# Kernel tuning notes

Hardware: AMD Instinct MI355X
Metric: run time of the kernel (lower is better)

The kernel has to match this reference:

```python
import jax, jax.numpy as jnp
import numpy as np

D_MODEL, N_HEAD, D_HEAD = 1024, 16, 64
BATCH, Q_LEN = 2, 2048
LN_EPS = 1e-5


def _rel_shift(x):
    # x: [b, q, k, n] -- standard Transformer-XL relative shift
    b, q, k, n = x.shape
    zero_pad = jnp.zeros((b, q, 1, n), dtype=x.dtype)
    x_padded = jnp.concatenate([zero_pad, x], axis=2)      # [b, q, k+1, n]
    x_padded = x_padded.reshape(b, k + 1, q, n)
    return x_padded[:, 1:].reshape(b, q, k, n)


def _layer_norm(x, gamma, beta):
    mu = jnp.mean(x, axis=-1, keepdims=True)
    var = jnp.mean(jnp.square(x - mu), axis=-1, keepdims=True)
    return (x - mu) * jax.lax.rsqrt(var + LN_EPS) * gamma + beta


def setup_inputs() -> dict:
    key = jax.random.key(0)
    ks = jax.random.split(key, 8)
    inp = {
        "x": jax.random.normal(ks[0], (BATCH, Q_LEN, D_MODEL), jnp.float32),
        "relative_pos": jax.random.normal(ks[1], (Q_LEN, D_MODEL), jnp.float32),
        "r_w_bias": jax.random.normal(ks[2], (N_HEAD, D_HEAD), jnp.float32) * 0.02,
        "r_r_bias": jax.random.normal(ks[3], (N_HEAD, D_HEAD), jnp.float32) * 0.02,
        "attn_mask": jax.random.randint(ks[4], (BATCH, Q_LEN), 0, 2).astype(bool),
        "W_qkv": jax.random.normal(ks[5], (D_MODEL, 3 * N_HEAD * D_HEAD), jnp.float32) / np.sqrt(D_MODEL),
        "W_rel": jax.random.normal(ks[6], (D_MODEL, N_HEAD * D_HEAD), jnp.float32) / np.sqrt(D_MODEL),
        "W_out": jax.random.normal(ks[7], (N_HEAD * D_HEAD, D_MODEL), jnp.float32) / np.sqrt(N_HEAD * D_HEAD),
        "ln_gamma": jnp.ones((D_MODEL,), jnp.float32),
        "ln_beta": jnp.zeros((D_MODEL,), jnp.float32),
    }
    return inp


def reference(x, relative_pos, r_w_bias, r_r_bias, attn_mask, W_qkv, W_rel, W_out, ln_gamma, ln_beta):
    b, q_len, _ = x.shape
    r_len = relative_pos.shape[0]
    scale = 1.0 / np.sqrt(D_HEAD)

    w_heads = x @ W_qkv                                    # [b, q, 3*n*d]
    w_q, w_k, w_v = jnp.split(w_heads, 3, axis=-1)
    k_len = w_k.shape[1]

    w_q = w_q.reshape(b, q_len, N_HEAD, D_HEAD)
    w_k = w_k.reshape(b, k_len, N_HEAD, D_HEAD)
    w_v = w_v.reshape(b, k_len, N_HEAD, D_HEAD)
    r_k = (relative_pos @ W_rel).reshape(r_len, N_HEAD, D_HEAD)

    rw_q = w_q + r_w_bias                                  # [b, q, n, d]
    rr_q = w_q + r_r_bias

    ac = jnp.einsum('bind,bjnd->bijn', rw_q, w_k)          # content score
    bd = jnp.einsum('bind,jnd->bijn', rr_q, r_k)           # position score
    bd = _rel_shift(bd)

    attn_score = (ac + bd) * scale                         # [b, q, k, n]
    attn_score = jnp.where(attn_mask[:, None, :, None], -jnp.inf, attn_score)
    attn_prob = jax.nn.softmax(attn_score, axis=2)

    context = jnp.einsum('bijn,bjnd->bind', attn_prob, w_v)
    context = context.reshape(b, q_len, N_HEAD * D_HEAD)
    attn_out = context @ W_out
    return _layer_norm(x + attn_out, ln_gamma, ln_beta)
```

## Files before the change

### kernel.cpp

```cpp
#include <hip/hip_runtime.h>
#include <hip/hip_bf16.h>
#include <math.h>

#define S_LEN 2048
#define NHEAD 16
#define DHEAD 64
#define DMODEL 1024
#define NBATCH 2

typedef unsigned short u16;
typedef __attribute__((ext_vector_type(8))) short bf16x8;
typedef __attribute__((ext_vector_type(4))) short short4v;
typedef __attribute__((ext_vector_type(4))) float f32x4;

__device__ __forceinline__ short f2bs(float x) {
    __hip_bfloat16 h = __float2bfloat16(x);
    return __builtin_bit_cast(short, h);
}

#define GL2LDS(g, l)                                                         \
    __builtin_amdgcn_global_load_lds(                                        \
        (const __attribute__((address_space(1))) void*)(g),                  \
        (__attribute__((address_space(3))) void*)(l), 16, 0, 0)

__global__ __launch_bounds__(256) void cast_f32_bf16(const float* __restrict__ in,
                                                     u16* __restrict__ out) {
    const int i = (blockIdx.x * 256 + threadIdx.x) * 4;
    float4 v = *(const float4*)(in + i);
    short4v t;
    t[0] = f2bs(v.x); t[1] = f2bs(v.y); t[2] = f2bs(v.z); t[3] = f2bs(v.w);
    *(short4v*)(out + i) = t;
}

__global__ __launch_bounds__(256) void transp_cast(const float* __restrict__ W,
                                                   u16* __restrict__ Wt,
                                                   int K, int N) {
    __shared__ float t[64][65];
    const int k0 = blockIdx.y * 64, n0 = blockIdx.x * 64;
    const int r = threadIdx.x >> 4;
    const int c4 = (threadIdx.x & 15) * 4;
    #pragma unroll
    for (int it = 0; it < 4; ++it) {
        float4 v = *(const float4*)(W + (size_t)(k0 + it * 16 + r) * N + n0 + c4);
        t[c4 + 0][it * 16 + r] = v.x;
        t[c4 + 1][it * 16 + r] = v.y;
        t[c4 + 2][it * 16 + r] = v.z;
        t[c4 + 3][it * 16 + r] = v.w;
    }
    __syncthreads();
    #pragma unroll
    for (int it = 0; it < 4; ++it) {
        const int nn = it * 16 + r;
        short4v o;
        o[0] = f2bs(t[nn][c4 + 0]); o[1] = f2bs(t[nn][c4 + 1]);
        o[2] = f2bs(t[nn][c4 + 2]); o[3] = f2bs(t[nn][c4 + 3]);
        *(short4v*)(Wt + (size_t)(n0 + nn) * K + k0 + c4) = o;
    }
}

#define GEMM_BODY(Aptr, Btptr, Kdim)                                          \
    __shared__ u16 As[128 * 64];                                              \
    __shared__ u16 Bs[128 * 64];                                              \
    const int tid = threadIdx.x;                                              \
    const int lane = tid & 63;                                                \
    const int w = tid >> 6;                                                   \
    const int quad = lane >> 4, col = lane & 15;                              \
    const int bm = blockIdx.y * 128, bn = blockIdx.x * 128;                   \
    const int wm = (w >> 1) * 64, wn = (w & 1) * 64;                          \
    f32x4 acc[4][4];                                                          \
    _Pragma("unroll")                                                         \
    for (int mt = 0; mt < 4; ++mt)                                            \
        _Pragma("unroll")                                                     \
        for (int nt = 0; nt < 4; ++nt) acc[mt][nt] = (f32x4){0.f,0.f,0.f,0.f};\
    for (int k0 = 0; k0 < (Kdim); k0 += 64) {                                 \
        _Pragma("unroll")                                                     \
        for (int it = 0; it < 4; ++it) {                                      \
            const int cb = it * 256 + w * 64;                                 \
            const int c = cb + lane;                                          \
            const int r = c >> 3;                                             \
            const int o = ((c & 7) ^ (r & 7)) * 8;                            \
            GL2LDS((Aptr) + (size_t)(bm + r) * (Kdim) + k0 + o, As + (size_t)cb * 8); \
            GL2LDS((Btptr) + (size_t)(bn + r) * (Kdim) + k0 + o, Bs + (size_t)cb * 8);\
        }                                                                     \
        __syncthreads();                                                      \
        _Pragma("unroll")                                                     \
        for (int kc = 0; kc < 2; ++kc) {                                      \
            bf16x8 af[4], bfr[4];                                             \
            _Pragma("unroll")                                                 \
            for (int t = 0; t < 4; ++t) {                                     \
                const int am = wm + t * 16 + col;                             \
                const int aj = kc * 4 + quad;                                 \
                af[t] = *(const bf16x8*)&As[(size_t)am * 64 + ((aj ^ (am & 7)) * 8)]; \
                const int bn2 = wn + t * 16 + col;                            \
                bfr[t] = *(const bf16x8*)&Bs[(size_t)bn2 * 64 + ((aj ^ (bn2 & 7)) * 8)]; \
            }                                                                 \
            _Pragma("unroll")                                                 \
            for (int mt = 0; mt < 4; ++mt)                                    \
                _Pragma("unroll")                                             \
                for (int nt = 0; nt < 4; ++nt)                                \
                    acc[mt][nt] = __builtin_amdgcn_mfma_f32_16x16x32_bf16(    \
                        af[mt], bfr[nt], acc[mt][nt], 0, 0, 0);               \
        }                                                                     \
        __syncthreads();                                                      \
    }

__global__ __launch_bounds__(256, 2) void gemm_qkv(
    const u16* __restrict__ A, const u16* __restrict__ Bt,
    const float* __restrict__ rwb, const float* __restrict__ rrb,
    u16* __restrict__ qrw_b, u16* __restrict__ qrr_b,
    u16* __restrict__ kb, u16* __restrict__ vbT)
{
    GEMM_BODY(A, Bt, DMODEL)
    #pragma unroll
    for (int mt = 0; mt < 4; ++mt) {
        const int row0 = bm + wm + mt * 16 + quad * 4;
        const int b = row0 >> 11;
        const int s0 = row0 & 2047;
        #pragma unroll
        for (int nt = 0; nt < 4; ++nt) {
            const int cn = bn + wn + nt * 16 + col;
            const int sec = cn >> 10;
            const int cc = cn & 1023;
            const int h = cc >> 6, d = cc & 63;
            const int bh = b * NHEAD + h;
            if (sec == 0) {
                const float bw = rwb[cc], br = rrb[cc];
                #pragma unroll
                for (int r = 0; r < 4; ++r) {
                    const size_t o = ((size_t)bh * S_LEN + s0 + r) * 64 + d;
                    qrw_b[o] = (u16)f2bs(acc[mt][nt][r] + bw);
                    qrr_b[o] = (u16)f2bs(acc[mt][nt][r] + br);
                }
            } else if (sec == 1) {
                #pragma unroll
                for (int r = 0; r < 4; ++r)
                    kb[((size_t)bh * S_LEN + s0 + r) * 64 + d] =
                        (u16)f2bs(acc[mt][nt][r]);
            } else {
                short4v t;
                t[0] = f2bs(acc[mt][nt][0]); t[1] = f2bs(acc[mt][nt][1]);
                t[2] = f2bs(acc[mt][nt][2]); t[3] = f2bs(acc[mt][nt][3]);
                *(short4v*)(vbT + ((size_t)bh * 64 + d) * S_LEN + s0) = t;
            }
        }
    }
}

__global__ __launch_bounds__(256, 2) void gemm_rel(
    const u16* __restrict__ A, const u16* __restrict__ Bt,
    u16* __restrict__ rkb)
{
    GEMM_BODY(A, Bt, DMODEL)
    #pragma unroll
    for (int mt = 0; mt < 4; ++mt) {
        const int l0 = bm + wm + mt * 16 + quad * 4;
        #pragma unroll
        for (int nt = 0; nt < 4; ++nt) {
            const int cn = bn + wn + nt * 16 + col;
            const int h = cn >> 6, d = cn & 63;
            #pragma unroll
            for (int r = 0; r < 4; ++r)
                rkb[((size_t)h * S_LEN + l0 + r) * 64 + d] =
                    (u16)f2bs(acc[mt][nt][r]);
        }
    }
}

__global__ __launch_bounds__(256, 2) void gemm_out(
    const u16* __restrict__ A, const u16* __restrict__ Bt,
    float* __restrict__ Cf, int N, int K)
{
    GEMM_BODY(A, Bt, K)
    #pragma unroll
    for (int mt = 0; mt < 4; ++mt)
        #pragma unroll
        for (int nt = 0; nt < 4; ++nt)
            #pragma unroll
            for (int r = 0; r < 4; ++r) {
                const int row = bm + wm + mt * 16 + quad * 4 + r;
                const int cn = bn + wn + nt * 16 + col;
                Cf[(size_t)row * N + cn] = acc[mt][nt][r];
            }
}

__global__ __launch_bounds__(512, 2) void flash_attn(
    const u16* __restrict__ qrw_b, const u16* __restrict__ qrr_b,
    const u16* __restrict__ kb, const u16* __restrict__ vbT,
    const u16* __restrict__ rkb, const int* __restrict__ mask,
    u16* __restrict__ ctxb)
{
    const int lane = threadIdx.x & 63;
    const int w    = threadIdx.x >> 6;
    const int quad = lane >> 4;
    const int col  = lane & 15;
    const int bh   = blockIdx.y;
    const int b    = bh >> 4;
    const int n    = bh & 15;
    const int B0   = blockIdx.x * 128;
    const int iw0  = B0 + w * 16;

    __shared__ u16 Ks[64 * 64];
    __shared__ u16 Vs[64 * 64];
    __shared__ u16 Rs[192 * 64];
    __shared__ u16 Pr[8][16][72];
    __shared__ float madd[S_LEN];

    const size_t headQ = (size_t)bh * S_LEN * 64;
    const size_t headR = (size_t)n  * S_LEN * 64;

    for (int i = threadIdx.x; i < S_LEN; i += 512)
        madd[i] = mask[b * S_LEN + i] ? -16384.f : 0.f;

    bf16x8 a_rw[2], a_rr0[2], a_rr1[2];
    {
        const int r0 = iw0 + col;
        const int r1 = (r0 + 1 < S_LEN) ? (r0 + 1) : (S_LEN - 1);
        #pragma unroll
        for (int kc = 0; kc < 2; ++kc) {
            const int doff = kc * 32 + quad * 8;
            a_rw[kc]  = *(const bf16x8*)(qrw_b + headQ + (size_t)r0 * 64 + doff);
            a_rr0[kc] = *(const bf16x8*)(qrr_b + headQ + (size_t)r0 * 64 + doff);
            a_rr1[kc] = *(const bf16x8*)(qrr_b + headQ + (size_t)r1 * 64 + doff);
        }
    }

    f32x4 O[4];
    float l_acc[4] = {0.f, 0.f, 0.f, 0.f};
    #pragma unroll
    for (int dt = 0; dt < 4; ++dt) O[dt] = (f32x4){0.f, 0.f, 0.f, 0.f};

    const int swz  = ((lane & 7) ^ ((lane >> 3) & 7)) * 8;
    const int lrow = lane >> 3;
    const int csel = col & 7;
    const int delta = B0 - 0 + 16 * w;

    for (int u0 = 0; u0 < S_LEN; u0 += 64) {
        const int dblk = B0 - u0;
        const int dw = dblk + 16 * w;
        const bool mixed = (dw >= 0) && (dw <= 48);
        __syncthreads();
        const int pbase = (dblk >= 0) ? (S_LEN - 128 - dblk) : (-dblk - 129);
        #pragma unroll
        for (int t = 0; t < 5; ++t) {
            const int idx = w * 5 + t;
            if (idx < 8) {
                GL2LDS(kb + headQ + (size_t)(u0 + idx * 8 + lrow) * 64 + swz,
                       Ks + idx * 512);
            } else if (idx < 16) {
                const int c = idx - 8;
                GL2LDS(vbT + ((size_t)bh * 64 + c * 8 + lrow) * S_LEN + u0 + swz,
                       Vs + c * 512);
            } else {
                const int c = idx - 16;
                int rr = pbase + c * 8 + lrow;
                rr = rr < 0 ? 0 : (rr > S_LEN - 1 ? S_LEN - 1 : rr);
                GL2LDS(rkb + headR + (size_t)rr * 64 + swz, Rs + c * 512);
            }
        }
        bf16x8 rf2[5][2];
        if (mixed) {
            #pragma unroll
            for (int g = 0; g < 5; ++g) {
                const int u = g * 16 + col;
                int row = (dblk >= 0) ? (u - dw - 17) : (S_LEN - 16 - dw + u);
                row = row < 0 ? 0 : (row > S_LEN - 1 ? S_LEN - 1 : row);
                const u16* rb = rkb + headR + (size_t)row * 64 + quad * 8;
                rf2[g][0] = *(const bf16x8*)(rb);
                rf2[g][1] = *(const bf16x8*)(rb + 32);
            }
        }
        __syncthreads();

        f32x4 sc[4];
        #pragma unroll
        for (int nt = 0; nt < 4; ++nt) {
            const int m = nt * 16 + col;
            bf16x8 k0 = *(const bf16x8*)&Ks[m * 64 + ((quad ^ csel) * 8)];
            bf16x8 k1 = *(const bf16x8*)&Ks[m * 64 + (((4 + quad) ^ csel) * 8)];
            f32x4 c = (f32x4){0.f, 0.f, 0.f, 0.f};
            c = __builtin_amdgcn_mfma_f32_16x16x32_bf16(a_rw[0], k0, c, 0, 0, 0);
            c = __builtin_amdgcn_mfma_f32_16x16x32_bf16(a_rw[1], k1, c, 0, 0, 0);
            sc[nt] = c;
        }

        f32x4 pnl[5], oth[5];
        {
            const bf16x8* aP = (dblk >= 0) ? a_rr0 : a_rr1;
            #pragma unroll
            for (int g = 0; g < 5; ++g) {
                const int m = g * 16 + col + 112 - 16 * w;
                bf16x8 r0 = *(const bf16x8*)&Rs[m * 64 + ((quad ^ csel) * 8)];
                bf16x8 r1 = *(const bf16x8*)&Rs[m * 64 + (((4 + quad) ^ csel) * 8)];
                f32x4 c = (f32x4){0.f, 0.f, 0.f, 0.f};
                c = __builtin_amdgcn_mfma_f32_16x16x32_bf16(aP[0], r0, c, 0, 0, 0);
                c = __builtin_amdgcn_mfma_f32_16x16x32_bf16(aP[1], r1, c, 0, 0, 0);
                pnl[g] = c;
            }
        }
        #pragma unroll
        for (int g = 0; g < 5; ++g) oth[g] = (f32x4){0.f, 0.f, 0.f, 0.f};
        if (mixed) {
            const bf16x8* aV = (dblk >= 0) ? a_rr1 : a_rr0;
            #pragma unroll
            for (int g = 0; g < 5; ++g) {
                f32x4 c = (f32x4){0.f, 0.f, 0.f, 0.f};
                c = __builtin_amdgcn_mfma_f32_16x16x32_bf16(aV[0], rf2[g][0], c, 0, 0, 0);
                c = __builtin_amdgcn_mfma_f32_16x16x32_bf16(aV[1], rf2[g][1], c, 0, 0, 0);
                oth[g] = c;
            }
        }
        const int lim1 = 15 + dw;
        #pragma unroll
        for (int g = 0; g < 5; ++g) {
            const int u = g * 16 + col;
            #pragma unroll
            for (int r = 0; r < 4; ++r) {
                const float r1v = (dblk >= 0) ? pnl[g][r] : oth[g][r];
                const float r2v = (dblk >= 0) ? oth[g][r] : pnl[g][r];
                pnl[g][r] = (u <= lim1) ? r1v : ((u == lim1 + 1) ? 0.f : r2v);
            }
        }

        #pragma unroll
        for (int nt = 0; nt < 4; ++nt) {
            const float ma = madd[u0 + nt * 16 + col];
            #pragma unroll
            for (int r = 0; r < 4; ++r) {
                const int uo = col + 15 - quad * 4 - r;
                const int src = (quad << 4) | (uo & 15);
                float blo = __shfl(pnl[nt][r], src, 64);
                float bhi = __shfl(pnl[nt + 1][r], src, 64);
                float bd = (uo < 16) ? blo : bhi;
                float p = __expf(fmaf(sc[nt][r] + bd, 0.125f, ma));
                sc[nt][r] = p;
                l_acc[r] += p;
            }
        }

        #pragma unroll
        for (int nt = 0; nt < 4; ++nt)
            #pragma unroll
            for (int r = 0; r < 4; ++r)
                Pr[w][quad * 4 + r][nt * 16 + col] = (u16)f2bs(sc[nt][r]);
        bf16x8 pa[2];
        pa[0] = *(const bf16x8*)&Pr[w][col][quad * 8];
        pa[1] = *(const bf16x8*)&Pr[w][col][32 + quad * 8];

        #pragma unroll
        for (int dt = 0; dt < 4; ++dt) {
            const int m = dt * 16 + col;
            bf16x8 v0 = *(const bf16x8*)&Vs[m * 64 + ((quad ^ csel) * 8)];
            bf16x8 v1 = *(const bf16x8*)&Vs[m * 64 + (((4 + quad) ^ csel) * 8)];
            f32x4 c = O[dt];
            c = __builtin_amdgcn_mfma_f32_16x16x32_bf16(pa[0], v0, c, 0, 0, 0);
            c = __builtin_amdgcn_mfma_f32_16x16x32_bf16(pa[1], v1, c, 0, 0, 0);
            O[dt] = c;
        }
    }

    float inv[4];
    #pragma unroll
    for (int r = 0; r < 4; ++r) {
        float s = l_acc[r];
        #pragma unroll
        for (int off = 1; off < 16; off <<= 1)
            s += __shfl_xor(s, off, 64);
        inv[r] = 1.f / s;
    }
    #pragma unroll
    for (int dt = 0; dt < 4; ++dt)
        #pragma unroll
        for (int r = 0; r < 4; ++r) {
            const int i = iw0 + quad * 4 + r;
            ctxb[((size_t)b * S_LEN + i) * DMODEL + n * 64 + dt * 16 + col] =
                (u16)f2bs(O[dt][r] * inv[r]);
        }
}

__global__ __launch_bounds__(256) void ln_kernel(const float* __restrict__ x,
                                                 const float* __restrict__ ao,
                                                 const float* __restrict__ gamma,
                                                 const float* __restrict__ beta,
                                                 float* __restrict__ out) {
    const int r = blockIdx.x;
    const int tid = threadIdx.x;
    const size_t base = (size_t)r * DMODEL + tid * 4;
    float4 xv = *(const float4*)(x + base);
    float4 av = *(const float4*)(ao + base);
    float v0 = xv.x + av.x, v1 = xv.y + av.y, v2 = xv.z + av.z, v3 = xv.w + av.w;

    float s = v0 + v1 + v2 + v3;
    #pragma unroll
    for (int off = 32; off > 0; off >>= 1) s += __shfl_xor(s, off, 64);
    __shared__ float red[4];
    __shared__ float red2[4];
    if ((tid & 63) == 0) red[tid >> 6] = s;
    __syncthreads();
    float mu = (red[0] + red[1] + red[2] + red[3]) * (1.0f / DMODEL);

    float d0 = v0 - mu, d1 = v1 - mu, d2 = v2 - mu, d3 = v3 - mu;
    float q = d0 * d0 + d1 * d1 + d2 * d2 + d3 * d3;
    #pragma unroll
    for (int off = 32; off > 0; off >>= 1) q += __shfl_xor(q, off, 64);
    if ((tid & 63) == 0) red2[tid >> 6] = q;
    __syncthreads();
    float var = (red2[0] + red2[1] + red2[2] + red2[3]) * (1.0f / DMODEL);
    float rstd = rsqrtf(var + 1e-5f);

    float4 g  = *(const float4*)(gamma + tid * 4);
    float4 be = *(const float4*)(beta + tid * 4);
    float4 o = make_float4(d0 * rstd * g.x + be.x,
                           d1 * rstd * g.y + be.y,
                           d2 * rstd * g.z + be.z,
                           d3 * rstd * g.w + be.w);
    *(float4*)(out + base) = o;
}

extern "C" void kernel_launch(void* const* d_in, const int* in_sizes, int n_in,
                              void* d_out, int out_size, void* d_ws, size_t ws_size,
                              hipStream_t stream) {
    const float* x    = (const float*)d_in[0];
    const float* rpos = (const float*)d_in[1];
    const float* rwb  = (const float*)d_in[2];
    const float* rrb  = (const float*)d_in[3];
    const int*   mask = (const int*)  d_in[4];
    const float* Wqkv = (const float*)d_in[5];
    const float* Wrel = (const float*)d_in[6];
    const float* Wout = (const float*)d_in[7];
    const float* gam  = (const float*)d_in[8];
    const float* bet  = (const float*)d_in[9];
    float* out = (float*)d_out;

    u16* wsb   = (u16*)d_ws;
    u16* ctxb  = wsb;
    float* ao  = (float*)(wsb + 4194304);
    u16* qrw_b = wsb + 12582912;
    u16* qrr_b = qrw_b + 4194304;
    u16* kb    = qrr_b + 4194304;
    u16* vbT   = kb + 4194304;
    u16* rkb   = vbT + 4194304;
    u16* xb    = rkb + 2097152;
    u16* rposb = xb + 4194304;
    u16* Wqkvt = rposb + 2097152;
    u16* Wrelt = Wqkvt + 3145728;
    u16* Woutt = Wrelt + 1048576;

    dim3 blk(256);
    cast_f32_bf16<<<dim3(4096), blk, 0, stream>>>(x, xb);
    transp_cast<<<dim3(48, 16), blk, 0, stream>>>(Wqkv, Wqkvt, DMODEL, 3 * DMODEL);
    gemm_qkv<<<dim3(24, 32), blk, 0, stream>>>(xb, Wqkvt, rwb, rrb,
                                               qrw_b, qrr_b, kb, vbT);
    cast_f32_bf16<<<dim3(2048), blk, 0, stream>>>(rpos, rposb);
    transp_cast<<<dim3(16, 16), blk, 0, stream>>>(Wrel, Wrelt, DMODEL, DMODEL);
    gemm_rel<<<dim3(8, 16), blk, 0, stream>>>(rposb, Wrelt, rkb);
    transp_cast<<<dim3(16, 16), blk, 0, stream>>>(Wout, Woutt, DMODEL, DMODEL);
    flash_attn<<<dim3(S_LEN / 128, NBATCH * NHEAD), dim3(512), 0, stream>>>(
        qrw_b, qrr_b, kb, vbT, rkb, mask, ctxb);
    gemm_out<<<dim3(8, 32), blk, 0, stream>>>(ctxb, Woutt, ao, DMODEL, DMODEL);
    ln_kernel<<<dim3(NBATCH * S_LEN), blk, 0, stream>>>(x, ao, gam, bet, out);
}
```

Baseline: 350.2 us.

## Load V tiles directly into registers and deduplicate rel-shift shuffles

V is no longer staged through shared memory. Each wave now reads its V^T fragments from global memory straight into registers, and the LDS staging loop shrinks from 5 to 4 chunks per wave. The rel-shift shuffle loop is also reordered so each pnl group is shuffled once per row instead of twice (5 shuffles instead of 8). The mask values are hoisted into registers. This cuts LDS footprint and traffic and DS-permute work, at the cost of redundant global/L2 reads of V across the 8 waves and extra register pressure.

```diff
diff --git a/kernel.cpp b/kernel.cpp
--- a/kernel.cpp
+++ b/kernel.cpp
@@ -200,7 +200,6 @@
     const int iw0  = B0 + w * 16;
 
     __shared__ u16 Ks[64 * 64];
-    __shared__ u16 Vs[64 * 64];
     __shared__ u16 Rs[192 * 64];
     __shared__ u16 Pr[8][16][72];
     __shared__ float madd[S_LEN];
@@ -232,7 +231,6 @@
     const int swz  = ((lane & 7) ^ ((lane >> 3) & 7)) * 8;
     const int lrow = lane >> 3;
     const int csel = col & 7;
-    const int delta = B0 - 0 + 16 * w;
 
     for (int u0 = 0; u0 < S_LEN; u0 += 64) {
         const int dblk = B0 - u0;
@@ -241,17 +239,13 @@
         __syncthreads();
         const int pbase = (dblk >= 0) ? (S_LEN - 128 - dblk) : (-dblk - 129);
         #pragma unroll
-        for (int t = 0; t < 5; ++t) {
-            const int idx = w * 5 + t;
+        for (int t = 0; t < 4; ++t) {
+            const int idx = w * 4 + t;
             if (idx < 8) {
                 GL2LDS(kb + headQ + (size_t)(u0 + idx * 8 + lrow) * 64 + swz,
                        Ks + idx * 512);
-            } else if (idx < 16) {
+            } else {
                 const int c = idx - 8;
-                GL2LDS(vbT + ((size_t)bh * 64 + c * 8 + lrow) * S_LEN + u0 + swz,
-                       Vs + c * 512);
-            } else {
-                const int c = idx - 16;
                 int rr = pbase + c * 8 + lrow;
                 rr = rr < 0 ? 0 : (rr > S_LEN - 1 ? S_LEN - 1 : rr);
                 GL2LDS(rkb + headR + (size_t)rr * 64 + swz, Rs + c * 512);
@@ -321,17 +315,31 @@
             }
         }
 
-        #pragma unroll
-        for (int nt = 0; nt < 4; ++nt) {
-            const float ma = madd[u0 + nt * 16 + col];
-            #pragma unroll
-            for (int r = 0; r < 4; ++r) {
-                const int uo = col + 15 - quad * 4 - r;
-                const int src = (quad << 4) | (uo & 15);
-                float blo = __shfl(pnl[nt][r], src, 64);
-                float bhi = __shfl(pnl[nt + 1][r], src, 64);
-                float bd = (uo < 16) ? blo : bhi;
-                float p = __expf(fmaf(sc[nt][r] + bd, 0.125f, ma));
+        bf16x8 vf[4][2];
+        #pragma unroll
+        for (int dt = 0; dt < 4; ++dt) {
+            const u16* vb = vbT + ((size_t)bh * 64 + dt * 16 + col) * S_LEN
+                            + u0 + quad * 8;
+            vf[dt][0] = *(const bf16x8*)(vb);
+            vf[dt][1] = *(const bf16x8*)(vb + 32);
+        }
+
+        float madd_v[4];
+        #pragma unroll
+        for (int nt = 0; nt < 4; ++nt)
+            madd_v[nt] = madd[u0 + nt * 16 + col];
+        #pragma unroll
+        for (int r = 0; r < 4; ++r) {
+            const int uo = col + 15 - quad * 4 - r;
+            const int src = (quad << 4) | (uo & 15);
+            float rot[5];
+            #pragma unroll
+            for (int g = 0; g < 5; ++g)
+                rot[g] = __shfl(pnl[g][r], src, 64);
+            #pragma unroll
+            for (int nt = 0; nt < 4; ++nt) {
+                const float bd = (uo < 16) ? rot[nt] : rot[nt + 1];
+                const float p = __expf(fmaf(sc[nt][r] + bd, 0.125f, madd_v[nt]));
                 sc[nt][r] = p;
                 l_acc[r] += p;
             }
@@ -348,12 +356,9 @@
 
         #pragma unroll
         for (int dt = 0; dt < 4; ++dt) {
-            const int m = dt * 16 + col;
-            bf16x8 v0 = *(const bf16x8*)&Vs[m * 64 + ((quad ^ csel) * 8)];
-            bf16x8 v1 = *(const bf16x8*)&Vs[m * 64 + (((4 + quad) ^ csel) * 8)];
             f32x4 c = O[dt];
-            c = __builtin_amdgcn_mfma_f32_16x16x32_bf16(pa[0], v0, c, 0, 0, 0);
-            c = __builtin_amdgcn_mfma_f32_16x16x32_bf16(pa[1], v1, c, 0, 0, 0);
+            c = __builtin_amdgcn_mfma_f32_16x16x32_bf16(pa[0], vf[dt][0], c, 0, 0, 0);
+            c = __builtin_amdgcn_mfma_f32_16x16x32_bf16(pa[1], vf[dt][1], c, 0, 0, 0);
             O[dt] = c;
         }
     }
```

New measurement: 463.7 us. 1.32x slower.
